# Optimization experiments

Measured on AMD Instinct MI355X. Metric: run time of the kernel, lower is better.

The kernel has to match this reference:

```python
import jax, jax.numpy as jnp
import numpy as np

B, SQ, SK, HID, H, D = 2, 2048, 2048, 1024, 16, 64
LN_EPS = 1e-12


def _sinusoid(seq_len):
    # [1,1,S,D]: first half sin, second half cos (RoFormer convention)
    pos = np.arange(seq_len, dtype=np.float32)[:, None]
    inv_freq = 1.0 / (10000.0 ** (np.arange(0, D, 2, dtype=np.float32) / D))
    ang = pos * inv_freq  # [S, D/2]
    return jnp.asarray(np.concatenate([np.sin(ang), np.cos(ang)], axis=-1)[None, None], dtype=jnp.float32)


def setup_inputs() -> dict:
    key = jax.random.key(0)
    ks = jax.random.split(key, 12)
    w = lambda k, shape: jax.random.normal(k, shape, dtype=jnp.float32) * 0.02
    return {
        "hidden_states": jax.random.normal(ks[0], (B, SQ, HID), dtype=jnp.float32),
        "encoder_hidden_states": jax.random.normal(ks[1], (B, SK, HID), dtype=jnp.float32),
        "encoder_attention_mask": jnp.zeros((B, 1, 1, SK), dtype=jnp.float32),  # additive mask
        "sinusoidal_pos": _sinusoid(SQ),
        "c_sinusoidal_pos": _sinusoid(SK),
        "Wq": w(ks[2], (HID, HID)), "bq": jnp.zeros((HID,), jnp.float32),
        "Wk": w(ks[3], (HID, HID)), "bk": jnp.zeros((HID,), jnp.float32),
        "Wv": w(ks[4], (HID, HID)), "bv": jnp.zeros((HID,), jnp.float32),
        "Wd": w(ks[5], (HID, HID)), "bd": jnp.zeros((HID,), jnp.float32),
        "ln_gamma": jnp.ones((HID,), jnp.float32),
        "ln_beta": jnp.zeros((HID,), jnp.float32),
    }


def apply_rope(sinusoidal_pos, layer):
    # sinusoidal_pos: [1,1,S,D] = sin||cos halves; layer: [B,H,S,D]
    sin, cos = jnp.split(sinusoidal_pos, 2, axis=-1)
    sin_pos = jnp.stack([sin, sin], axis=-1).reshape(sinusoidal_pos.shape)
    cos_pos = jnp.stack([cos, cos], axis=-1).reshape(sinusoidal_pos.shape)
    rot = jnp.stack([-layer[..., 1::2], layer[..., ::2]], axis=-1).reshape(layer.shape)
    return layer * cos_pos + rot * sin_pos


def _heads(x):
    b, s, _ = x.shape
    return x.reshape(b, s, H, D).transpose(0, 2, 1, 3)  # [B,H,S,D]


def reference(hidden_states, encoder_hidden_states, encoder_attention_mask,
              sinusoidal_pos, c_sinusoidal_pos,
              Wq, bq, Wk, bk, Wv, bv, Wd, bd, ln_gamma, ln_beta):
    q = _heads(hidden_states @ Wq.T + bq)
    k = _heads(encoder_hidden_states @ Wk.T + bk)
    v = _heads(encoder_hidden_states @ Wv.T + bv)
    q = apply_rope(sinusoidal_pos, q)
    k = apply_rope(c_sinusoidal_pos, k)

    scores = jnp.einsum("bhqd,bhkd->bhqk", q, k) / jnp.sqrt(jnp.float32(D))
    scores = scores + encoder_attention_mask  # broadcast [B,1,1,SK]
    probs = jax.nn.softmax(scores, axis=-1)
    ctx = jnp.einsum("bhqk,bhkd->bhqd", probs, v)
    ctx = ctx.transpose(0, 2, 1, 3).reshape(hidden_states.shape[0], -1, HID)

    proj = ctx @ Wd.T + bd
    x = hidden_states + proj
    mu = jnp.mean(x, axis=-1, keepdims=True)
    var = jnp.mean(jnp.square(x - mu), axis=-1, keepdims=True)
    return (x - mu) / jnp.sqrt(var + LN_EPS) * ln_gamma + ln_beta
```

## Files before the change

### kernel.cpp

```cpp
#include <hip/hip_runtime.h>

typedef __attribute__((ext_vector_type(8))) short short8;
typedef __attribute__((ext_vector_type(4))) float f32x4;
typedef __attribute__((ext_vector_type(16))) float f32x16;

#define LOG2E 1.4426950408889634f
#define QSCALE 0.18033688011112042f

#define ASM_VMCNT4() asm volatile("s_waitcnt vmcnt(4)" ::: "memory")
#define ASM_VMCNT0() asm volatile("s_waitcnt vmcnt(0)" ::: "memory")
#define ASM_LGKM0()  asm volatile("s_waitcnt lgkmcnt(0)" ::: "memory")

static __device__ __forceinline__ unsigned short f2bf(float f){
  unsigned u = __builtin_bit_cast(unsigned, f);
  u += 0x7FFFu + ((u>>16)&1u);
  return (unsigned short)(u>>16);
}

static __device__ __forceinline__ void async16(const void* g, const void* l){
  __builtin_amdgcn_global_load_lds(
      (const __attribute__((address_space(1))) unsigned*)(unsigned long long)g,
      (__attribute__((address_space(3))) unsigned*)(unsigned)(unsigned long long)l,
      16, 0, 0);
}

__global__ __launch_bounds__(256) void prep_kernel(
    const float* __restrict__ hidden, unsigned short* __restrict__ hb,
    const float* __restrict__ encoder, unsigned short* __restrict__ eb,
    const float* __restrict__ Wq, unsigned short* __restrict__ wqb,
    const float* __restrict__ Wk, unsigned short* __restrict__ wkb,
    const float* __restrict__ Wv, unsigned short* __restrict__ wvb,
    const float* __restrict__ Wd, unsigned short* __restrict__ wdb,
    const float* __restrict__ mask, float* __restrict__ maskE)
{
  int blk = blockIdx.x;
  if (blk < 6144){
    const float* src; unsigned short* dst; int i;
    if (blk < 4096){
      int t = blk*256 + threadIdx.x;
      src = (t >> 19) ? encoder : hidden;
      dst = (t >> 19) ? eb : hb;
      i = (t & 524287)*8;
    } else {
      int t = (blk-4096)*256 + threadIdx.x;
      int z = t >> 17;
      src = (z==0)?Wq:(z==1)?Wk:(z==2)?Wv:Wd;
      dst = (z==0)?wqb:(z==1)?wkb:(z==2)?wvb:wdb;
      i = (t & 131071)*8;
    }
    const float4* s4 = (const float4*)(src + i);
    float4 a = s4[0], b = s4[1];
    union { unsigned short u[8]; short8 v; } o;
    o.u[0]=f2bf(a.x); o.u[1]=f2bf(a.y); o.u[2]=f2bf(a.z); o.u[3]=f2bf(a.w);
    o.u[4]=f2bf(b.x); o.u[5]=f2bf(b.y); o.u[6]=f2bf(b.z); o.u[7]=f2bf(b.w);
    *(short8*)(dst + i) = o.v;
  } else {
    int i = (blk-6144)*256 + threadIdx.x;
    float4 v = ((const float4*)mask)[i];
    v.x*=LOG2E; v.y*=LOG2E; v.z*=LOG2E; v.w*=LOG2E;
    ((float4*)maskE)[i] = v;
  }
}

__global__ __launch_bounds__(256) void gemm_qkv(
    const unsigned short* __restrict__ hb, const unsigned short* __restrict__ eb,
    const unsigned short* __restrict__ wqb, const unsigned short* __restrict__ wkb,
    const unsigned short* __restrict__ wvb,
    const float* __restrict__ bq, const float* __restrict__ bk, const float* __restrict__ bv,
    const float* __restrict__ sp, const float* __restrict__ csp,
    unsigned short* __restrict__ Qb, unsigned short* __restrict__ Kb, unsigned short* __restrict__ Vt)
{
  const int z = blockIdx.z;
  const unsigned short* A = (z==0) ? hb : eb;
  const unsigned short* W = (z==0) ? wqb : (z==1 ? wkb : wvb);
  const float* bias = (z==0) ? bq : (z==1 ? bk : bv);
  const float* rope = (z==0) ? sp : (z==1 ? csp : nullptr);

  __shared__ unsigned short As[2][128*32];
  __shared__ unsigned short Bs[2][128*32];

  const int tid = threadIdx.x;
  const int w = tid>>6, l = tid&63;
  const int bm = blockIdx.y, bn = blockIdx.x;
  const int wr = w>>1, wc = w&1;

  const f32x4 zero = {0.f,0.f,0.f,0.f};
  f32x4 acc[4][4];
  #pragma unroll
  for (int m=0;m<4;m++)
    #pragma unroll
    for (int n=0;n<4;n++) acc[m][n] = zero;

  auto stage = [&](int buf, int kt){
    #pragma unroll
    for (int j=0;j<2;j++){
      int c = w*2 + j;
      int e0 = c*512 + l*8;
      int row = e0>>5, col = e0&31;
      async16(A + (size_t)(bm*128 + row)*1024 + kt*32 + col, As[buf] + e0);
      async16(W + (size_t)(bn*128 + row)*1024 + kt*32 + col, Bs[buf] + e0);
    }
  };

  stage(0, 0);

  for (int kt=0; kt<32; ++kt){
    int cur = kt&1;
    if (kt < 31){ stage(cur^1, kt+1); ASM_VMCNT4(); }
    else        { ASM_VMCNT0(); }
    __builtin_amdgcn_s_barrier();
    __builtin_amdgcn_sched_barrier(0);

    short8 af[4], bf[4];
    #pragma unroll
    for (int m=0;m<4;m++)
      af[m] = *(const short8*)(As[cur] + (wr*64 + m*16 + (l&15))*32 + (l>>4)*8);
    #pragma unroll
    for (int n=0;n<4;n++)
      bf[n] = *(const short8*)(Bs[cur] + (wc*64 + n*16 + (l&15))*32 + (l>>4)*8);
    #pragma unroll
    for (int m=0;m<4;m++)
      #pragma unroll
      for (int n=0;n<4;n++)
        acc[m][n] = __builtin_amdgcn_mfma_f32_16x16x32_bf16(af[m], bf[n], acc[m][n], 0,0,0);

    ASM_LGKM0();
    __builtin_amdgcn_s_barrier();
  }

  if (z == 2){
    #pragma unroll
    for (int m=0;m<4;m++){
      #pragma unroll
      for (int n=0;n<4;n++){
        int mr0 = bm*128 + wr*64 + m*16 + (l>>4)*4;
        int nc  = bn*128 + wc*64 + n*16 + (l&15);
        int b0 = mr0>>11, s0 = mr0&2047;
        int h = nc>>6, d = nc&63;
        float bia = bias[nc];
        union { unsigned short u[4]; unsigned long long ull; } pk;
        #pragma unroll
        for (int r=0;r<4;r++) pk.u[r] = f2bf(acc[m][n][r] + bia);
        *(unsigned long long*)(Vt + ((size_t)(b0*16 + h)*64 + d)*2048 + s0) = pk.ull;
      }
    }
  } else {
    #pragma unroll
    for (int m=0;m<4;m++){
      #pragma unroll
      for (int n=0;n<4;n++){
        #pragma unroll
        for (int r=0;r<4;r++){
          int mr = bm*128 + wr*64 + m*16 + (l>>4)*4 + r;
          int nc = bn*128 + wc*64 + n*16 + (l&15);
          float v = acc[m][n][r] + bias[nc];
          int b = mr>>11, s = mr&2047;
          int h = nc>>6,  d = nc&63;
          float p = __shfl_xor(v, 1);
          float sv = rope[s*64 + (d>>1)];
          float cv = rope[s*64 + 32 + (d>>1)];
          float ov = (d&1) ? (v*cv + p*sv) : (v*cv - p*sv);
          if (z == 0) ov *= QSCALE;
          unsigned short* out = (z==0) ? Qb : Kb;
          out[((size_t)(b*16 + h)*2048 + s)*64 + d] = f2bf(ov);
        }
      }
    }
  }
}

__global__ __launch_bounds__(512) void flash_attn(
    const unsigned short* __restrict__ Qb, const unsigned short* __restrict__ Kb,
    const unsigned short* __restrict__ Vt, const float* __restrict__ maskE,
    unsigned short* __restrict__ ctx)
{
  __shared__ unsigned short Kls[2][2][4096];
  __shared__ unsigned short Vls[2][2][4096];
  __shared__ float maskLS[2048];

  const int tid = threadIdx.x;
  const int w = tid>>6, l = tid&63;
  const int qc = l&31, hi = l>>5;
  const int wq = w&3, half = w>>2;

  const int flat = blockIdx.x;
  const int o = (flat&7)*64 + (flat>>3);
  const int qt = o&15, bh = o>>4;
  const int b = bh>>4, h = bh&15;

  {
    ((float4*)maskLS)[tid] = ((const float4*)(maskE + b*2048))[tid];
  }

  const int qrow = qt*128 + wq*32 + qc;
  const unsigned short* qptr = Qb + ((size_t)bh*2048 + qrow)*64;
  short8 qf[4];
  #pragma unroll
  for (int ks=0;ks<4;ks++) qf[ks] = *(const short8*)(qptr + ks*16 + hi*8);

  float m_r = -1e30f, l_r = 0.f;
  f32x16 oacc[2];
  #pragma unroll
  for (int t3=0;t3<2;t3++)
    #pragma unroll
    for (int i=0;i<16;i++) oacc[t3][i] = 0.f;

  const int srow = l>>3;
  const int scol = ((l&7) ^ srow)*8;
  const unsigned short* kSrc0; const unsigned short* kSrc1;
  const unsigned short* vSrc0; const unsigned short* vSrc1;
  {
    int c0 = wq*2, c1 = wq*2+1;
    kSrc0 = Kb + ((size_t)bh*2048 + half*1024 + c0*8 + srow)*64 + scol;
    kSrc1 = Kb + ((size_t)bh*2048 + half*1024 + c1*8 + srow)*64 + scol;
    vSrc0 = Vt + ((size_t)bh*64 + c0*8 + srow)*2048 + half*1024 + scol;
    vSrc1 = Vt + ((size_t)bh*64 + c1*8 + srow)*2048 + half*1024 + scol;
  }
  const int ld0 = (wq*2)*512 + l*8, ld1 = (wq*2+1)*512 + l*8;

  auto stage = [&](int buf){
    async16(kSrc0, &Kls[half][buf][ld0]);
    async16(kSrc1, &Kls[half][buf][ld1]);
    async16(vSrc0, &Vls[half][buf][ld0]);
    async16(vSrc1, &Vls[half][buf][ld1]);
    kSrc0 += 4096; kSrc1 += 4096;
    vSrc0 += 64;   vSrc1 += 64;
  };

  stage(0);
  ASM_LGKM0();
  int cur = 0;

  const int rg0 = (qc&7);

  for (int ktl=0; ktl<16; ++ktl){
    if (ktl < 15){ stage(cur^1); ASM_VMCNT4(); }
    else         { ASM_VMCNT0(); }
    __builtin_amdgcn_s_barrier();
    __builtin_amdgcn_sched_barrier(0);

    f32x16 sacc[2];
    #pragma unroll
    for (int t2=0;t2<2;t2++)
      #pragma unroll
      for (int i=0;i<16;i++) sacc[t2][i] = 0.f;

    __builtin_amdgcn_s_setprio(1);
    #pragma unroll
    for (int ks=0; ks<4; ++ks){
      const short8 kf0 = *(const short8*)(&Kls[half][cur][ qc*64      + (((ks*2+hi)^rg0)*8) ]);
      const short8 kf1 = *(const short8*)(&Kls[half][cur][ (32+qc)*64 + (((ks*2+hi)^rg0)*8) ]);
      sacc[0] = __builtin_amdgcn_mfma_f32_32x32x16_bf16(kf0, qf[ks], sacc[0], 0,0,0);
      sacc[1] = __builtin_amdgcn_mfma_f32_32x32x16_bf16(kf1, qf[ks], sacc[1], 0,0,0);
    }
    __builtin_amdgcn_s_setprio(0);

    float rm = -1e30f;
    #pragma unroll
    for (int t2=0;t2<2;t2++){
      #pragma unroll
      for (int rg=0;rg<4;rg++){
        const float4 mv = *(const float4*)&maskLS[half*1024 + ktl*64 + t2*32 + rg*8 + hi*4];
        float s0 = sacc[t2][rg*4+0] + mv.x;
        float s1 = sacc[t2][rg*4+1] + mv.y;
        float s2 = sacc[t2][rg*4+2] + mv.z;
        float s3 = sacc[t2][rg*4+3] + mv.w;
        sacc[t2][rg*4+0]=s0; sacc[t2][rg*4+1]=s1; sacc[t2][rg*4+2]=s2; sacc[t2][rg*4+3]=s3;
        rm = fmaxf(fmaxf(rm, s0), fmaxf(fmaxf(s1, s2), s3));
      }
    }
    { float a = rm, c2 = rm;
      asm("v_permlane32_swap_b32 %0, %1" : "+v"(a), "+v"(c2));
      rm = fmaxf(a, c2); }

    bool keep = __all(rm <= m_r + 8.0f);
    float mnew = keep ? m_r : fmaxf(m_r, rm);
    float rs = 0.f;
    #pragma unroll
    for (int t2=0;t2<2;t2++)
      #pragma unroll
      for (int i=0;i<16;i++){
        float e = __builtin_amdgcn_exp2f(sacc[t2][i] - mnew);
        sacc[t2][i] = e;
        rs += e;
      }
    { float a = rs, c2 = rs;
      asm("v_permlane32_swap_b32 %0, %1" : "+v"(a), "+v"(c2));
      rs = a + c2; }
    if (keep){
      l_r += rs;
    } else {
      float scl = __builtin_amdgcn_exp2f(m_r - mnew);
      l_r = l_r*scl + rs;
      m_r = mnew;
      #pragma unroll
      for (int t3=0;t3<2;t3++)
        #pragma unroll
        for (int i=0;i<16;i++) oacc[t3][i] *= scl;
    }

    short8 pB[4];
    #pragma unroll
    for (int t2=0;t2<2;t2++){
      #pragma unroll
      for (int hf=0; hf<2; ++hf){
        unsigned x0,x1,x2,x3;
        asm("v_cvt_pk_bf16_f32 %0, %1, %2" : "=v"(x0) : "v"(sacc[t2][hf*8+0]), "v"(sacc[t2][hf*8+1]));
        asm("v_cvt_pk_bf16_f32 %0, %1, %2" : "=v"(x1) : "v"(sacc[t2][hf*8+2]), "v"(sacc[t2][hf*8+3]));
        asm("v_cvt_pk_bf16_f32 %0, %1, %2" : "=v"(x2) : "v"(sacc[t2][hf*8+4]), "v"(sacc[t2][hf*8+5]));
        asm("v_cvt_pk_bf16_f32 %0, %1, %2" : "=v"(x3) : "v"(sacc[t2][hf*8+6]), "v"(sacc[t2][hf*8+7]));
        asm("v_permlane32_swap_b32 %0, %1" : "+v"(x2), "+v"(x0));
        asm("v_permlane32_swap_b32 %0, %1" : "+v"(x3), "+v"(x1));
        union { unsigned u[4]; short8 v; } pb;
        pb.u[0]=x0; pb.u[1]=x1; pb.u[2]=x2; pb.u[3]=x3;
        pB[t2*2+hf] = pb.v;
      }
    }

    __builtin_amdgcn_s_setprio(1);
    #pragma unroll
    for (int t3=0;t3<2;t3++){
      #pragma unroll
      for (int si=0; si<4; ++si){
        const short8 vf = *(const short8*)(&Vls[half][cur][ (t3*32+qc)*64 + (((si*2+hi)^rg0)*8) ]);
        oacc[t3] = __builtin_amdgcn_mfma_f32_32x32x16_bf16(vf, pB[si], oacc[t3], 0,0,0);
      }
    }
    __builtin_amdgcn_s_setprio(0);

    ASM_LGKM0();
    __builtin_amdgcn_s_barrier();
    cur ^= 1;
  }

  float* Ox  = (float*)&Kls[0][0][0];
  float* MLf = (float*)&Vls[0][0][0];

  if (half == 1){
    #pragma unroll
    for (int t3=0;t3<2;t3++){
      #pragma unroll
      for (int rg=0;rg<4;rg++){
        int dbase = t3*32 + rg*8 + hi*4;
        f32x4 o4 = { oacc[t3][rg*4+0], oacc[t3][rg*4+1], oacc[t3][rg*4+2], oacc[t3][rg*4+3] };
        *(f32x4*)&Ox[wq*2048 + qc*64 + (dbase ^ (rg0*8))] = o4;
      }
    }
    if (hi == 0){
      MLf[wq*64 + qc]      = m_r;
      MLf[wq*64 + 32 + qc] = l_r;
    }
  }
  __syncthreads();

  if (half == 0){
    float m1 = MLf[wq*64 + qc];
    float l1 = MLf[wq*64 + 32 + qc];
    float mstar = fmaxf(m_r, m1);
    float s0 = __builtin_amdgcn_exp2f(m_r - mstar);
    float s1 = __builtin_amdgcn_exp2f(m1 - mstar);
    float inv = 1.0f / (l_r*s0 + l1*s1);
    float a0 = s0*inv, a1 = s1*inv;

    int qglob = qt*128 + wq*32 + qc;
    unsigned short* cp = ctx + ((size_t)b*2048 + qglob)*1024 + h*64;
    #pragma unroll
    for (int t3=0;t3<2;t3++){
      #pragma unroll
      for (int rg=0;rg<4;rg++){
        int dbase = t3*32 + rg*8 + hi*4;
        f32x4 o1 = *(const f32x4*)&Ox[wq*2048 + qc*64 + (dbase ^ (rg0*8))];
        union { unsigned short u[4]; unsigned long long ull; } pk4;
        #pragma unroll
        for (int i=0;i<4;i++) pk4.u[i] = f2bf(oacc[t3][rg*4+i]*a0 + o1[i]*a1);
        *(unsigned long long*)(cp + dbase) = pk4.ull;
      }
    }
  }
}

__global__ __launch_bounds__(256) void gemm_proj(
    const unsigned short* __restrict__ ctxb, const unsigned short* __restrict__ wdb,
    const float* __restrict__ bd, const float* __restrict__ hidden,
    float* __restrict__ X)
{
  __shared__ unsigned short As[2][128*32];
  __shared__ unsigned short Bs[2][128*32];
  const int tid = threadIdx.x;
  const int w = tid>>6, l = tid&63;
  const int bm = blockIdx.y, bn = blockIdx.x;
  const int wr = w>>1, wc = w&1;

  const f32x4 zero = {0.f,0.f,0.f,0.f};
  f32x4 acc[4][4];
  #pragma unroll
  for (int m=0;m<4;m++)
    #pragma unroll
    for (int n=0;n<4;n++) acc[m][n] = zero;

  auto stage = [&](int buf, int kt){
    #pragma unroll
    for (int j=0;j<2;j++){
      int c = w*2 + j;
      int e0 = c*512 + l*8;
      int row = e0>>5, col = e0&31;
      async16(ctxb + (size_t)(bm*128 + row)*1024 + kt*32 + col, As[buf] + e0);
      async16(wdb  + (size_t)(bn*128 + row)*1024 + kt*32 + col, Bs[buf] + e0);
    }
  };

  stage(0, 0);

  for (int kt=0; kt<32; ++kt){
    int cur = kt&1;
    if (kt < 31){ stage(cur^1, kt+1); ASM_VMCNT4(); }
    else        { ASM_VMCNT0(); }
    __builtin_amdgcn_s_barrier();
    __builtin_amdgcn_sched_barrier(0);

    short8 af[4], bf[4];
    #pragma unroll
    for (int m=0;m<4;m++)
      af[m] = *(const short8*)(As[cur] + (wr*64 + m*16 + (l&15))*32 + (l>>4)*8);
    #pragma unroll
    for (int n=0;n<4;n++)
      bf[n] = *(const short8*)(Bs[cur] + (wc*64 + n*16 + (l&15))*32 + (l>>4)*8);
    #pragma unroll
    for (int m=0;m<4;m++)
      #pragma unroll
      for (int n=0;n<4;n++)
        acc[m][n] = __builtin_amdgcn_mfma_f32_16x16x32_bf16(af[m], bf[n], acc[m][n], 0,0,0);

    ASM_LGKM0();
    __builtin_amdgcn_s_barrier();
  }

  #pragma unroll
  for (int m=0;m<4;m++){
    #pragma unroll
    for (int n=0;n<4;n++){
      #pragma unroll
      for (int r=0;r<4;r++){
        int mr = bm*128 + wr*64 + m*16 + (l>>4)*4 + r;
        int nc = bn*128 + wc*64 + n*16 + (l&15);
        float v = acc[m][n][r] + bd[nc] + hidden[(size_t)mr*1024 + nc];
        X[(size_t)mr*1024 + nc] = v;
      }
    }
  }
}

__global__ __launch_bounds__(256) void ln_kernel(
    const float* __restrict__ X, const float* __restrict__ gamma,
    const float* __restrict__ beta, float* __restrict__ out)
{
  const int row = blockIdx.x;
  const int tid = threadIdx.x;
  const float4 v = ((const float4*)(X + (size_t)row*1024))[tid];
  float s  = v.x+v.y+v.z+v.w;
  float ss = v.x*v.x + v.y*v.y + v.z*v.z + v.w*v.w;
  #pragma unroll
  for (int off=1; off<64; off<<=1){
    s  += __shfl_xor(s, off);
    ss += __shfl_xor(ss, off);
  }
  __shared__ float red[8];
  const int w = tid>>6, l = tid&63;
  if (l == 0){ red[w] = s; red[4+w] = ss; }
  __syncthreads();
  s  = red[0]+red[1]+red[2]+red[3];
  ss = red[4]+red[5]+red[6]+red[7];
  float mu  = s*(1.f/1024.f);
  float var = ss*(1.f/1024.f) - mu*mu;
  float inv = rsqrtf(var + 1e-12f);
  const float4 g  = ((const float4*)gamma)[tid];
  const float4 bt = ((const float4*)beta)[tid];
  float4 o;
  o.x = (v.x-mu)*inv*g.x + bt.x;
  o.y = (v.y-mu)*inv*g.y + bt.y;
  o.z = (v.z-mu)*inv*g.z + bt.z;
  o.w = (v.w-mu)*inv*g.w + bt.w;
  ((float4*)(out + (size_t)row*1024))[tid] = o;
}

extern "C" void kernel_launch(void* const* d_in, const int* in_sizes, int n_in,
                              void* d_out, int out_size, void* d_ws, size_t ws_size,
                              hipStream_t stream) {
  const float* hidden  = (const float*)d_in[0];
  const float* encoder = (const float*)d_in[1];
  const float* mask    = (const float*)d_in[2];
  const float* sp      = (const float*)d_in[3];
  const float* csp     = (const float*)d_in[4];
  const float* Wq = (const float*)d_in[5];  const float* bq = (const float*)d_in[6];
  const float* Wk = (const float*)d_in[7];  const float* bk = (const float*)d_in[8];
  const float* Wv = (const float*)d_in[9];  const float* bv = (const float*)d_in[10];
  const float* Wd = (const float*)d_in[11]; const float* bd = (const float*)d_in[12];
  const float* gamma = (const float*)d_in[13];
  const float* beta  = (const float*)d_in[14];

  char* ws = (char*)d_ws;
  const size_t MB_ = 1ull<<20;
  unsigned short* hb  = (unsigned short*)(ws + 0);
  unsigned short* eb  = (unsigned short*)(ws + 8*MB_);
  unsigned short* wqb = (unsigned short*)(ws + 16*MB_);
  unsigned short* wkb = (unsigned short*)(ws + 18*MB_);
  unsigned short* wvb = (unsigned short*)(ws + 20*MB_);
  unsigned short* wdb = (unsigned short*)(ws + 22*MB_);
  unsigned short* Qb  = (unsigned short*)(ws + 24*MB_);
  unsigned short* Kb  = (unsigned short*)(ws + 32*MB_);
  unsigned short* Vt  = (unsigned short*)(ws + 40*MB_);
  unsigned short* ctxb = hb;
  float* X = (float*)(ws + 24*MB_);
  float* maskE = (float*)(ws + 48*MB_);

  prep_kernel<<<6148,256,0,stream>>>(hidden, hb, encoder, eb,
                                     Wq, wqb, Wk, wkb, Wv, wvb, Wd, wdb,
                                     mask, maskE);

  gemm_qkv<<<dim3(8,32,3),256,0,stream>>>(hb, eb, wqb, wkb, wvb,
                                          bq, bk, bv, sp, csp, Qb, Kb, Vt);
  flash_attn<<<512,512,0,stream>>>(Qb, Kb, Vt, maskE, ctxb);
  gemm_proj<<<dim3(8,32),256,0,stream>>>(ctxb, wdb, bd, hidden, X);
  ln_kernel<<<4096,256,0,stream>>>(X, gamma, beta, (float*)d_out);
}
```

Baseline: 150.5 us.

## Drop per-tile running max; fold mask into MFMA accumulator init; simplify barriers

The per-tile row-max reduction and max-update logic are removed from the online softmax. Scores are exponentiated against a fixed running offset (starting at 0), and a rare fallback rescales only when the row sum would overflow. The additive mask is now loaded as the initial accumulator of the QK MFMA, which removes a separate add pass. The explicit vmcnt waits and raw barriers are replaced by __syncthreads, which waits on all outstanding loads including the just-issued prefetch and can reduce load/compute overlap. The fixed offset also risks overflow or underflow if the score range grows large.

New measurement: 138.8 us. 7.8% less time.

```diff
diff --git a/kernel.cpp b/kernel.cpp
--- a/kernel.cpp
+++ b/kernel.cpp
@@ -198,7 +198,7 @@
   #pragma unroll
   for (int ks=0;ks<4;ks++) qf[ks] = *(const short8*)(qptr + ks*16 + hi*8);
 
-  float m_r = -1e30f, l_r = 0.f;
+  float m_r = 0.f, l_r = 0.f;
   f32x16 oacc[2];
   #pragma unroll
   for (int t3=0;t3<2;t3++)
@@ -228,22 +228,26 @@
   };
 
   stage(0);
-  ASM_LGKM0();
+  __syncthreads();
   int cur = 0;
 
   const int rg0 = (qc&7);
 
   for (int ktl=0; ktl<16; ++ktl){
-    if (ktl < 15){ stage(cur^1); ASM_VMCNT4(); }
-    else         { ASM_VMCNT0(); }
-    __builtin_amdgcn_s_barrier();
-    __builtin_amdgcn_sched_barrier(0);
+    if (ktl < 15) stage(cur^1);
 
     f32x16 sacc[2];
     #pragma unroll
-    for (int t2=0;t2<2;t2++)
-      #pragma unroll
-      for (int i=0;i<16;i++) sacc[t2][i] = 0.f;
+    for (int t2=0;t2<2;t2++){
+      #pragma unroll
+      for (int rg=0;rg<4;rg++){
+        const float4 mv = *(const float4*)&maskLS[half*1024 + ktl*64 + t2*32 + rg*8 + hi*4];
+        sacc[t2][rg*4+0] = mv.x;
+        sacc[t2][rg*4+1] = mv.y;
+        sacc[t2][rg*4+2] = mv.z;
+        sacc[t2][rg*4+3] = mv.w;
+      }
+    }
 
     __builtin_amdgcn_s_setprio(1);
     #pragma unroll
@@ -255,49 +259,42 @@
     }
     __builtin_amdgcn_s_setprio(0);
 
-    float rm = -1e30f;
-    #pragma unroll
-    for (int t2=0;t2<2;t2++){
-      #pragma unroll
-      for (int rg=0;rg<4;rg++){
-        const float4 mv = *(const float4*)&maskLS[half*1024 + ktl*64 + t2*32 + rg*8 + hi*4];
-        float s0 = sacc[t2][rg*4+0] + mv.x;
-        float s1 = sacc[t2][rg*4+1] + mv.y;
-        float s2 = sacc[t2][rg*4+2] + mv.z;
-        float s3 = sacc[t2][rg*4+3] + mv.w;
-        sacc[t2][rg*4+0]=s0; sacc[t2][rg*4+1]=s1; sacc[t2][rg*4+2]=s2; sacc[t2][rg*4+3]=s3;
-        rm = fmaxf(fmaxf(rm, s0), fmaxf(fmaxf(s1, s2), s3));
-      }
-    }
-    { float a = rm, c2 = rm;
-      asm("v_permlane32_swap_b32 %0, %1" : "+v"(a), "+v"(c2));
-      rm = fmaxf(a, c2); }
-
-    bool keep = __all(rm <= m_r + 8.0f);
-    float mnew = keep ? m_r : fmaxf(m_r, rm);
     float rs = 0.f;
     #pragma unroll
     for (int t2=0;t2<2;t2++)
       #pragma unroll
       for (int i=0;i<16;i++){
-        float e = __builtin_amdgcn_exp2f(sacc[t2][i] - mnew);
+        float e = __builtin_amdgcn_exp2f(sacc[t2][i] - m_r);
         sacc[t2][i] = e;
         rs += e;
       }
     { float a = rs, c2 = rs;
       asm("v_permlane32_swap_b32 %0, %1" : "+v"(a), "+v"(c2));
       rs = a + c2; }
-    if (keep){
-      l_r += rs;
-    } else {
-      float scl = __builtin_amdgcn_exp2f(m_r - mnew);
-      l_r = l_r*scl + rs;
-      m_r = mnew;
+
+    if (__builtin_expect(!__all(rs <= 16777216.0f), 0)){
+      float cm = 1.0f;
+      #pragma unroll
+      for (int t2=0;t2<2;t2++)
+        #pragma unroll
+        for (int i=0;i<16;i++) cm = fmaxf(cm, sacc[t2][i]);
+      { float a = cm, c2 = cm;
+        asm("v_permlane32_swap_b32 %0, %1" : "+v"(a), "+v"(c2));
+        cm = fmaxf(a, c2); }
+      float rin = 1.0f/cm;
+      #pragma unroll
+      for (int t2=0;t2<2;t2++)
+        #pragma unroll
+        for (int i=0;i<16;i++) sacc[t2][i] *= rin;
       #pragma unroll
       for (int t3=0;t3<2;t3++)
         #pragma unroll
-        for (int i=0;i<16;i++) oacc[t3][i] *= scl;
-    }
+        for (int i=0;i<16;i++) oacc[t3][i] *= rin;
+      l_r *= rin;
+      rs  *= rin;
+      m_r += log2f(cm);
+    }
+    l_r += rs;
 
     short8 pB[4];
     #pragma unroll
@@ -328,8 +325,7 @@
     }
     __builtin_amdgcn_s_setprio(0);
 
-    ASM_LGKM0();
-    __builtin_amdgcn_s_barrier();
+    __syncthreads();
     cur ^= 1;
   }
 
```
